# Performance work log

Hardware: AMD Instinct MI355X
Metric: run time of the kernel (lower is better)

The kernel has to match this reference:

```python
import jax, jax.numpy as jnp
import numpy as np

N = 100000   # nodes per graph-batch side
E = 1280000  # directed edges
G = 256      # graphs per batch
F_IN, HID, EMB = 64, 128, 64
BN_EPS = 1e-5


def setup_inputs() -> dict:
    key = jax.random.key(0)
    ks = jax.random.split(key, 24)
    inp = {}
    inp["x1"] = jax.random.normal(ks[0], (N, F_IN), dtype=jnp.float32)
    inp["x2"] = jax.random.normal(ks[1], (N, F_IN), dtype=jnp.float32)
    inp["edge_index1"] = jax.random.randint(ks[2], (2, E), 0, N, dtype=jnp.int64)
    inp["edge_index2"] = jax.random.randint(ks[3], (2, E), 0, N, dtype=jnp.int64)
    inp["batch1"] = jnp.sort(jax.random.randint(ks[4], (N,), 0, G, dtype=jnp.int64))
    inp["batch2"] = jnp.sort(jax.random.randint(ks[5], (N,), 0, G, dtype=jnp.int64))
    # shared (siamese) encoder parameters: 3 GIN layers (Linear+BN), final linear
    dims = [(F_IN, HID), (HID, HID), (HID, HID)]
    for i, (di, do) in enumerate(dims, 1):
        inp[f"W{i}"] = jax.random.normal(ks[5 + i], (di, do), dtype=jnp.float32) * (1.0 / np.sqrt(di))
        inp[f"b{i}"] = jnp.zeros((do,), dtype=jnp.float32)
        inp[f"g{i}"] = jnp.ones((do,), dtype=jnp.float32)   # BN gamma
        inp[f"be{i}"] = jnp.zeros((do,), dtype=jnp.float32)  # BN beta
    inp["Wf"] = jax.random.normal(ks[10], (HID, EMB), dtype=jnp.float32) * (1.0 / np.sqrt(HID))
    inp["bf"] = jnp.zeros((EMB,), dtype=jnp.float32)
    # classifier: Linear(EMB, HID//2) -> ReLU -> Linear(HID//2, 1) -> Sigmoid
    inp["Wc1"] = jax.random.normal(ks[11], (EMB, HID // 2), dtype=jnp.float32) * (1.0 / np.sqrt(EMB))
    inp["bc1"] = jnp.zeros((HID // 2,), dtype=jnp.float32)
    inp["Wc2"] = jax.random.normal(ks[12], (HID // 2, 1), dtype=jnp.float32) * (1.0 / np.sqrt(HID // 2))
    inp["bc2"] = jnp.zeros((1,), dtype=jnp.float32)
    return inp


def _gin_layer(x, src, dst, W, b, g, be):
    # GINConv eps=0: agg = x + sum_{j->i} x_j ; MLP = Linear -> BatchNorm1d -> ReLU
    agg = x + jax.ops.segment_sum(x[src], dst, num_segments=N)
    h = agg @ W + b
    mu = jnp.mean(h, axis=0)
    var = jnp.var(h, axis=0)
    h = (h - mu) * jax.lax.rsqrt(var + BN_EPS) * g + be
    return jax.nn.relu(h)  # MLP ReLU; outer .relu() in forward is idempotent


def _encode(x, edge_index, batch, Ws, bs, gs, bes, Wf, bf):
    src, dst = edge_index[0], edge_index[1]
    for W, b, g, be in zip(Ws, bs, gs, bes):
        x = _gin_layer(x, src, dst, W, b, g, be)
    # global_mean_pool
    sums = jax.ops.segment_sum(x, batch, num_segments=G)
    cnt = jax.ops.segment_sum(jnp.ones((N,), x.dtype), batch, num_segments=G)
    pooled = sums / jnp.maximum(cnt, 1.0)[:, None]
    return pooled @ Wf + bf


def reference(x1, edge_index1, batch1, x2, edge_index2, batch2,
              W1, b1, g1, be1, W2, b2, g2, be2, W3, b3, g3, be3,
              Wf, bf, Wc1, bc1, Wc2, bc2):
    Ws, bs, gs, bes = (W1, W2, W3), (b1, b2, b3), (g1, g2, g3), (be1, be2, be3)
    v1 = _encode(x1, edge_index1, batch1, Ws, bs, gs, bes, Wf, bf)
    v2 = _encode(x2, edge_index2, batch2, Ws, bs, gs, bes, Wf, bf)
    diff = jnp.abs(v1 - v2)
    h = jax.nn.relu(diff @ Wc1 + bc1)
    return jax.nn.sigmoid(h @ Wc2 + bc2)  # [G, 1]
```

## Files before the change

### kernel.cpp

```cpp
#include <hip/hip_runtime.h>
#include <hip/hip_bf16.h>
#include <math.h>

#define NN 100000
#define NE 1280000
#define NG 256
#define HID 128
#define EMB 64
#define BN_EPS 1e-5f
#define SB 1024
#define SNB ((NN + SB - 1) / SB)
#define GBLK 25000
#define NBG 1563
#define PART ((NN + 7) / 8)
#define FCH 2048
#define NCH (NE / FCH)

typedef __attribute__((ext_vector_type(8))) __bf16 bf16x8;
typedef __attribute__((ext_vector_type(4))) float f32x4;

__device__ __forceinline__ float bf2f(unsigned int u) { return __uint_as_float(u << 16); }
__device__ __forceinline__ unsigned int f2b(float f) {
    unsigned int u = __float_as_uint(f);
    return (u + 0x7fffu + ((u >> 16) & 1u)) >> 16;
}

__global__ void detect_i64_kernel(const void* __restrict__ ei, int* __restrict__ flag) {
    if (threadIdx.x == 0 && blockIdx.x == 0) {
        const unsigned long long* p = (const unsigned long long*)ei;
        int is64 = 1;
        #pragma unroll
        for (int i = 0; i < 16; ++i)
            if (p[i] >= (1ull << 32)) is64 = 0;
        *flag = is64;
    }
}

__device__ __forceinline__ int load_idx(const void* p, int i, bool is64) {
    return is64 ? (int)((const long long*)p)[i] : ((const int*)p)[i];
}

__global__ __launch_bounds__(256) void convert_x(const float* __restrict__ x1,
                                                 const float* __restrict__ x2,
                                                 ushort* __restrict__ o1,
                                                 ushort* __restrict__ o2) {
    const int per = NN * 16;
    const int i = blockIdx.x * 256 + threadIdx.x;
    const int side = i >= per;
    const int j = i - side * per;
    const float4 v = ((const float4*)(side ? x2 : x1))[j];
    ushort4 o;
    o.x = (ushort)f2b(v.x); o.y = (ushort)f2b(v.y);
    o.z = (ushort)f2b(v.z); o.w = (ushort)f2b(v.w);
    ((ushort4*)(side ? o2 : o1))[j] = o;
}

__global__ __launch_bounds__(256) void prep_weights(const float* __restrict__ W1,
                                                    const float* __restrict__ W2,
                                                    const float* __restrict__ W3,
                                                    ushort* __restrict__ T1,
                                                    ushort* __restrict__ T2,
                                                    ushort* __restrict__ T3) {
    const int i = blockIdx.x * 256 + threadIdx.x;
    if (i < 8192) {
        const int k = i >> 7, c = i & 127;
        T1[c * 64 + k] = (ushort)f2b(W1[i]);
    } else if (i < 24576) {
        const int j = i - 8192, k = j >> 7, c = j & 127;
        T2[c * 128 + k] = (ushort)f2b(W2[j]);
    } else if (i < 40960) {
        const int j = i - 24576, k = j >> 7, c = j & 127;
        T3[c * 128 + k] = (ushort)f2b(W3[j]);
    }
}

__global__ __launch_bounds__(256) void csr_hist2(const void* __restrict__ e1,
                                                 const void* __restrict__ e2,
                                                 int* __restrict__ degA,
                                                 int* __restrict__ degB,
                                                 const int* __restrict__ flag) {
    const bool is64 = (*flag != 0);
    const int i = blockIdx.x * 256 + threadIdx.x;
    if (i < 2 * NE) {
        const int side = i >= NE;
        const int j = i - side * NE;
        atomicAdd(&(side ? degB : degA)[load_idx(side ? e2 : e1, NE + j, is64)], 1);
    }
}

__global__ __launch_bounds__(256) void scan_block_sums2(const int* __restrict__ degA,
                                                        const int* __restrict__ degB,
                                                        int* __restrict__ bsum) {
    const int side = blockIdx.x >= SNB;
    const int bx = blockIdx.x - side * SNB;
    const int* deg = side ? degB : degA;
    const int t = threadIdx.x;
    const int base = bx * SB + t * 4;
    int s = 0;
    #pragma unroll
    for (int k = 0; k < 4; ++k) {
        const int i = base + k;
        if (i < NN) s += deg[i];
    }
    __shared__ int red[256];
    red[t] = s;
    __syncthreads();
    for (int off = 128; off > 0; off >>= 1) {
        if (t < off) red[t] += red[t + off];
        __syncthreads();
    }
    if (t == 0) bsum[side * 128 + bx] = red[0];
}

__global__ __launch_bounds__(128) void scan_bsums2(const int* __restrict__ bsum,
                                                   int* __restrict__ boff,
                                                   int* __restrict__ rpA,
                                                   int* __restrict__ rpB) {
    const int side = blockIdx.x;
    __shared__ int s[128];
    const int t = threadIdx.x;
    s[t] = (t < SNB) ? bsum[side * 128 + t] : 0;
    __syncthreads();
    for (int off = 1; off < 128; off <<= 1) {
        const int v = (t >= off) ? s[t - off] : 0;
        __syncthreads();
        s[t] += v;
        __syncthreads();
    }
    boff[side * 128 + t] = (t == 0) ? 0 : s[t - 1];
    if (t == 0) (side ? rpB : rpA)[NN] = s[SNB - 1];
}

__global__ __launch_bounds__(256) void scan_fill2(const int* __restrict__ degA,
                                                  const int* __restrict__ degB,
                                                  const int* __restrict__ boff,
                                                  int* __restrict__ rpA,
                                                  int* __restrict__ rpB,
                                                  int* __restrict__ curA,
                                                  int* __restrict__ curB) {
    const int side = blockIdx.x >= SNB;
    const int bx = blockIdx.x - side * SNB;
    const int* deg = side ? degB : degA;
    int* rowptr = side ? rpB : rpA;
    int* cursor = side ? curB : curA;
    const int t = threadIdx.x;
    const int base = bx * SB + t * 4;
    int v[4], s = 0;
    #pragma unroll
    for (int k = 0; k < 4; ++k) {
        const int i = base + k;
        v[k] = (i < NN) ? deg[i] : 0;
        s += v[k];
    }
    __shared__ int red[256];
    red[t] = s;
    __syncthreads();
    for (int off = 1; off < 256; off <<= 1) {
        const int x = (t >= off) ? red[t - off] : 0;
        __syncthreads();
        red[t] += x;
        __syncthreads();
    }
    int run = boff[side * 128 + bx] + ((t == 0) ? 0 : red[t - 1]);
    #pragma unroll
    for (int k = 0; k < 4; ++k) {
        const int i = base + k;
        if (i < NN) {
            rowptr[i] = run;
            cursor[i] = run;
            run += v[k];
        }
    }
}

__global__ __launch_bounds__(256) void csr_fill_part(const void* __restrict__ e1,
                                                     const void* __restrict__ e2,
                                                     int* __restrict__ curA,
                                                     int* __restrict__ curB,
                                                     int* __restrict__ colA,
                                                     int* __restrict__ colB,
                                                     const int* __restrict__ flag) {
    const bool is64 = (*flag != 0);
    const int g = blockIdx.x & 7;
    const int q = blockIdx.x >> 3;
    const int side = q >= NCH;
    const int chunk = q - side * NCH;
    const void* __restrict__ e = side ? e2 : e1;
    int* __restrict__ cur = side ? curB : curA;
    int* __restrict__ col = side ? colB : colA;
    const int lo = g * PART;
    const int hi = min(lo + PART, NN);
    const int base = chunk * FCH;
    for (int i = base + threadIdx.x; i < base + FCH; i += 256) {
        const int d = load_idx(e, NE + i, is64);
        if (d >= lo && d < hi) {
            const int pos = atomicAdd(&cur[d], 1);
            col[pos] = load_idx(e, i, is64);
        }
    }
}

struct GatherArgs {
    const ushort *xA, *xB;
    const int *rpA, *rpB, *colA, *colB;
    const float *stA, *stB;
    const float *gamma, *beta;
    ushort *oA, *oB;
};

template<int F, bool BN>
__global__ __launch_bounds__(256) void gather16(GatherArgs a) {
    const int side = blockIdx.x >= GBLK;
    const int bx = blockIdx.x - side * GBLK;
    const ushort* __restrict__ x = side ? a.xB : a.xA;
    const int* __restrict__ rowptr = side ? a.rpB : a.rpA;
    const int* __restrict__ col = side ? a.colB : a.colA;
    ushort* __restrict__ out = side ? a.oB : a.oA;

    const int node = (bx * 256 + threadIdx.x) >> 6;
    const int lane = threadIdx.x & 63;
    if (node >= NN) return;
    const int beg = rowptr[node], end = rowptr[node + 1];

    if (F == 64) {
        float acc = bf2f(x[node * 64 + lane]);
        int e = beg;
        for (; e + 3 < end; e += 4) {
            const int s0 = col[e], s1 = col[e + 1], s2 = col[e + 2], s3 = col[e + 3];
            acc += bf2f(x[s0 * 64 + lane]) + bf2f(x[s1 * 64 + lane])
                 + bf2f(x[s2 * 64 + lane]) + bf2f(x[s3 * 64 + lane]);
        }
        for (; e < end; ++e) acc += bf2f(x[col[e] * 64 + lane]);
        out[node * 64 + lane] = (ushort)f2b(acc);
    } else {
        float cax = 1.f, cay = 1.f, cbx = 0.f, cby = 0.f;
        if (BN) {
            const float* st = side ? a.stB : a.stA;
            const int c0 = lane * 2, c1 = c0 + 1;
            const float inv_n = 1.f / (float)NN;
            const float mu0 = st[c0] * inv_n, mu1 = st[c1] * inv_n;
            const float v0 = st[128 + c0] * inv_n - mu0 * mu0;
            const float v1 = st[128 + c1] * inv_n - mu1 * mu1;
            cax = a.gamma[c0] * rsqrtf(v0 + BN_EPS);
            cay = a.gamma[c1] * rsqrtf(v1 + BN_EPS);
            cbx = fmaf(-mu0, cax, a.beta[c0]);
            cby = fmaf(-mu1, cay, a.beta[c1]);
        }
        #define LD(s) (*(const unsigned int*)&x[(s) * 128 + lane * 2])
        #define FX(u) (BN ? fmaxf(fmaf(bf2f((u) & 0xffffu), cax, cbx), 0.f) : bf2f((u) & 0xffffu))
        #define FY(u) (BN ? fmaxf(fmaf(bf2f((u) >> 16),    cay, cby), 0.f) : bf2f((u) >> 16))
        const unsigned int u0 = LD(node);
        float ax = FX(u0), ay = FY(u0);
        int e = beg;
        for (; e + 3 < end; e += 4) {
            const unsigned int ua = LD(col[e]);
            const unsigned int ub = LD(col[e + 1]);
            const unsigned int uc = LD(col[e + 2]);
            const unsigned int ud = LD(col[e + 3]);
            ax += FX(ua) + FX(ub) + FX(uc) + FX(ud);
            ay += FY(ua) + FY(ub) + FY(uc) + FY(ud);
        }
        for (; e < end; ++e) {
            const unsigned int u = LD(col[e]);
            ax += FX(u); ay += FY(u);
        }
        #undef LD
        #undef FX
        #undef FY
        *(unsigned int*)&out[node * 128 + lane * 2] = f2b(ax) | (f2b(ay) << 16);
    }
}

struct GemmArgs {
    const ushort *mA, *mB;
    const ushort *WT;
    const float *bias;
    ushort *cA, *cB;
    float *stA, *stB;
};

template<int FIN>
__global__ __launch_bounds__(256) void gemm_mfma(GemmArgs g) {
    constexpr int FP = FIN + 8;
    constexpr int CPR = FIN / 8;
    const int side = blockIdx.x >= NBG;
    const int bx = blockIdx.x - side * NBG;
    const ushort* __restrict__ M = side ? g.mB : g.mA;
    ushort* __restrict__ C = side ? g.cB : g.cA;
    float* __restrict__ stats = side ? g.stB : g.stA;

    __shared__ ushort sh[64 * 136 + 128 * FP];
    ushort* Ml = sh;
    ushort* Wl = sh + 64 * 136;

    const int t = threadIdx.x;
    const int w = t >> 6;
    const int l = t & 63;
    const int lr = l & 15;
    const int lg = l >> 4;
    const int r0 = bx * 64;

    #pragma unroll
    for (int it = 0; it < (64 * CPR) / 256; ++it) {
        const int cid = it * 256 + t;
        const int row = cid / CPR, cc = (cid % CPR) * 8;
        const int r = r0 + row;
        uint4 v = make_uint4(0u, 0u, 0u, 0u);
        if (r < NN) v = *(const uint4*)&M[(size_t)r * FIN + cc];
        *(uint4*)&Ml[row * FP + cc] = v;
    }
    #pragma unroll
    for (int it = 0; it < (128 * CPR) / 256; ++it) {
        const int cid = it * 256 + t;
        const int c = cid / CPR, kk = (cid % CPR) * 8;
        *(uint4*)&Wl[c * FP + kk] = *(const uint4*)&g.WT[c * FIN + kk];
    }
    __syncthreads();

    f32x4 acc[4][2];
    #pragma unroll
    for (int fi = 0; fi < 4; ++fi)
        #pragma unroll
        for (int fj = 0; fj < 2; ++fj)
            acc[fi][fj] = (f32x4){0.f, 0.f, 0.f, 0.f};

    #pragma unroll
    for (int kc = 0; kc < FIN / 32; ++kc) {
        const int kb = kc * 32 + lg * 8;
        bf16x8 a[4], b[2];
        #pragma unroll
        for (int fi = 0; fi < 4; ++fi)
            a[fi] = *(const bf16x8*)&Ml[(fi * 16 + lr) * FP + kb];
        #pragma unroll
        for (int fj = 0; fj < 2; ++fj)
            b[fj] = *(const bf16x8*)&Wl[(w * 32 + fj * 16 + lr) * FP + kb];
        #pragma unroll
        for (int fi = 0; fi < 4; ++fi)
            #pragma unroll
            for (int fj = 0; fj < 2; ++fj)
                acc[fi][fj] = __builtin_amdgcn_mfma_f32_16x16x32_bf16(a[fi], b[fj], acc[fi][fj], 0, 0, 0);
    }
    __syncthreads();

    #pragma unroll
    for (int fj = 0; fj < 2; ++fj) {
        const float bv = g.bias[w * 32 + fj * 16 + lr];
        #pragma unroll
        for (int fi = 0; fi < 4; ++fi)
            #pragma unroll
            for (int j = 0; j < 4; ++j)
                acc[fi][fj][j] += bv;
    }
    #pragma unroll
    for (int fi = 0; fi < 4; ++fi)
        #pragma unroll
        for (int fj = 0; fj < 2; ++fj)
            #pragma unroll
            for (int j = 0; j < 4; ++j) {
                const int row = fi * 16 + lg * 4 + j;
                const int c = w * 32 + fj * 16 + lr;
                Ml[row * 136 + c] = (ushort)f2b(acc[fi][fj][j]);
            }
    __syncthreads();

    const int ry = t >> 4, c0 = (t & 15) * 8;
    float sc[8], qc[8];
    #pragma unroll
    for (int j = 0; j < 8; ++j) { sc[j] = 0.f; qc[j] = 0.f; }
    #pragma unroll
    for (int i = 0; i < 4; ++i) {
        const int rr = ry * 4 + i;
        const int r = r0 + rr;
        if (r < NN) {
            const uint4 pk = *(const uint4*)&Ml[rr * 136 + c0];
            const unsigned int uu[4] = {pk.x, pk.y, pk.z, pk.w};
            #pragma unroll
            for (int q = 0; q < 4; ++q) {
                const float e0 = bf2f(uu[q] & 0xffffu);
                const float e1 = bf2f(uu[q] >> 16);
                sc[2 * q] += e0;       sc[2 * q + 1] += e1;
                qc[2 * q] = fmaf(e0, e0, qc[2 * q]);
                qc[2 * q + 1] = fmaf(e1, e1, qc[2 * q + 1]);
            }
            *(uint4*)&C[(size_t)r * HID + c0] = pk;
        }
    }
    float* red = (float*)Wl;
    #pragma unroll
    for (int j = 0; j < 8; ++j) red[ry * 128 + c0 + j] = sc[j];
    __syncthreads();
    if (t < 128) {
        float a = 0.f;
        #pragma unroll
        for (int k = 0; k < 16; ++k) a += red[k * 128 + t];
        unsafeAtomicAdd(&stats[t], a);
    }
    __syncthreads();
    #pragma unroll
    for (int j = 0; j < 8; ++j) red[ry * 128 + c0 + j] = qc[j];
    __syncthreads();
    if (t < 128) {
        float a = 0.f;
        #pragma unroll
        for (int k = 0; k < 16; ++k) a += red[k * 128 + t];
        unsafeAtomicAdd(&stats[128 + t], a);
    }
}

struct PoolArgs {
    const ushort *hA, *hB;
    const void *btA, *btB;
    const float *stA, *stB;
    const float *gamma, *beta;
    float *pooled, *cnt;
    const int* flag;
};

__global__ __launch_bounds__(128) void pool16(PoolArgs p) {
    const int side = blockIdx.x >= NBG;
    const int bx = blockIdx.x - side * NBG;
    const ushort* __restrict__ h = side ? p.hB : p.hA;
    const void* __restrict__ batch = side ? p.btB : p.btA;
    const float* __restrict__ st = side ? p.stB : p.stA;
    float* pooled = p.pooled + side * NG * HID;
    float* cnt = p.cnt + side * NG;
    const bool is64 = (*p.flag != 0);
    const int c = threadIdx.x;

    const float inv_n = 1.f / (float)NN;
    const float mu = st[c] * inv_n;
    const float var = st[128 + c] * inv_n - mu * mu;
    const float ca = p.gamma[c] * rsqrtf(var + BN_EPS);
    const float cb = fmaf(-mu, ca, p.beta[c]);

    const int rbeg = bx * 64;
    if (rbeg >= NN) return;
    const int rend = min(rbeg + 64, NN);
    const int g0 = load_idx(batch, rbeg, is64);
    const int g1 = load_idx(batch, rend - 1, is64);
    if (g0 == g1) {
        float acc = 0.f;
        #pragma unroll 8
        for (int r = rbeg; r < rend; ++r)
            acc += fmaxf(fmaf(bf2f(h[r * HID + c]), ca, cb), 0.f);
        unsafeAtomicAdd(&pooled[g0 * HID + c], acc);
        if (c == 0) unsafeAtomicAdd(&cnt[g0], (float)(rend - rbeg));
        return;
    }
    int gprev = g0;
    float acc = 0.f; int run = 0;
    for (int r = rbeg; r < rend; ++r) {
        const int g = load_idx(batch, r, is64);
        if (g != gprev) {
            unsafeAtomicAdd(&pooled[gprev * HID + c], acc);
            if (c == 0) unsafeAtomicAdd(&cnt[gprev], (float)run);
            acc = 0.f; run = 0; gprev = g;
        }
        acc += fmaxf(fmaf(bf2f(h[r * HID + c]), ca, cb), 0.f);
        ++run;
    }
    unsafeAtomicAdd(&pooled[gprev * HID + c], acc);
    if (c == 0) unsafeAtomicAdd(&cnt[gprev], (float)run);
}

__global__ __launch_bounds__(64) void pool_proj(const float* __restrict__ pooled,
                                                const float* __restrict__ cnt,
                                                const float* __restrict__ Wf,
                                                const float* __restrict__ bf,
                                                float* __restrict__ v) {
    const int side = blockIdx.x >= NG;
    const int g = blockIdx.x - side * NG;
    const int c = threadIdx.x;
    const float* pp = pooled + side * NG * HID + g * HID;
    const float inv = 1.f / fmaxf(cnt[side * NG + g], 1.f);
    float acc = 0.f;
    for (int k = 0; k < HID; ++k) acc = fmaf(pp[k], Wf[k * EMB + c], acc);
    v[side * NG * EMB + g * EMB + c] = fmaf(acc, inv, bf[c]);
}

__global__ __launch_bounds__(256) void classifier(const float* __restrict__ v1,
                                                  const float* __restrict__ v2,
                                                  const float* __restrict__ Wc1,
                                                  const float* __restrict__ bc1,
                                                  const float* __restrict__ Wc2,
                                                  const float* __restrict__ bc2,
                                                  float* __restrict__ out) {
    const int g = threadIdx.x;
    if (g >= NG) return;
    float d[EMB];
    #pragma unroll
    for (int c = 0; c < EMB; ++c) d[c] = fabsf(v1[g * EMB + c] - v2[g * EMB + c]);
    float o = bc2[0];
    for (int j = 0; j < 32; ++j) {
        float h = bc1[j];
        #pragma unroll
        for (int c = 0; c < EMB; ++c) h = fmaf(d[c], Wc1[c * 32 + j], h);
        h = fmaxf(h, 0.f);
        o = fmaf(h, Wc2[j], o);
    }
    out[g] = 1.f / (1.f + expf(-o));
}

extern "C" void kernel_launch(void* const* d_in, const int* in_sizes, int n_in,
                              void* d_out, int out_size, void* d_ws, size_t ws_size,
                              hipStream_t stream) {
    const float* x1 = (const float*)d_in[0];
    const float* x2 = (const float*)d_in[1];
    const void* ei1 = d_in[2];
    const void* ei2 = d_in[3];
    const void* bt1 = d_in[4];
    const void* bt2 = d_in[5];
    const float* W[3]  = {(const float*)d_in[6],  (const float*)d_in[10], (const float*)d_in[14]};
    const float* bb[3] = {(const float*)d_in[7],  (const float*)d_in[11], (const float*)d_in[15]};
    const float* gg[3] = {(const float*)d_in[8],  (const float*)d_in[12], (const float*)d_in[16]};
    const float* be[3] = {(const float*)d_in[9],  (const float*)d_in[13], (const float*)d_in[17]};
    const float* Wf  = (const float*)d_in[18];
    const float* bfv = (const float*)d_in[19];
    const float* Wc1 = (const float*)d_in[20];
    const float* bc1 = (const float*)d_in[21];
    const float* Wc2 = (const float*)d_in[22];
    const float* bc2 = (const float*)d_in[23];

    char* cur = (char*)d_ws;
    auto alloc = [&](size_t bytes) -> void* {
        void* p = cur;
        cur += (bytes + 255) & ~(size_t)255;
        return p;
    };
    ushort* P0 = (ushort*)alloc((size_t)NN * HID * 2);
    ushort* P1 = (ushort*)alloc((size_t)NN * HID * 2);
    ushort* Q0 = (ushort*)alloc((size_t)NN * HID * 2);
    ushort* Q1 = (ushort*)alloc((size_t)NN * HID * 2);
    int* deg2   = (int*)alloc((size_t)2 * NN * 4);
    int* rpA    = (int*)alloc((size_t)(NN + 1) * 4);
    int* rpB    = (int*)alloc((size_t)(NN + 1) * 4);
    int* curA   = (int*)alloc((size_t)NN * 4);
    int* curB   = (int*)alloc((size_t)NN * 4);
    int* bsum   = (int*)alloc(256 * 4);
    int* boff   = (int*)alloc(256 * 4);
    int* colA   = (int*)alloc((size_t)NE * 4);
    int* colB   = (int*)alloc((size_t)NE * 4);
    int* flag   = (int*)alloc(64);
    ushort* WT1 = (ushort*)alloc(128 * 64 * 2);
    ushort* WT2 = (ushort*)alloc(128 * 128 * 2);
    ushort* WT3 = (ushort*)alloc(128 * 128 * 2);
    float* zreg = (float*)alloc((size_t)(6 * 256 + 2 * NG * HID + 2 * NG) * 4);
    float* stats  = zreg;
    float* pooled = stats + 6 * 256;
    float* cnt    = pooled + 2 * NG * HID;
    float* vv     = (float*)alloc((size_t)2 * NG * EMB * 4);
    int* degA = deg2, *degB = deg2 + NN;

    hipMemsetAsync(deg2, 0, (size_t)2 * NN * 4, stream);
    hipMemsetAsync(zreg, 0, (size_t)(6 * 256 + 2 * NG * HID + 2 * NG) * 4, stream);
    detect_i64_kernel<<<1, 64, 0, stream>>>(ei1, flag);
    convert_x<<<(2 * NN * 16) / 256, 256, 0, stream>>>(x1, x2, P0, P1);
    prep_weights<<<160, 256, 0, stream>>>(W[0], W[1], W[2], WT1, WT2, WT3);

    const int EB2 = (2 * NE + 255) / 256;
    csr_hist2<<<EB2, 256, 0, stream>>>(ei1, ei2, degA, degB, flag);
    scan_block_sums2<<<2 * SNB, 256, 0, stream>>>(degA, degB, bsum);
    scan_bsums2<<<2, 128, 0, stream>>>(bsum, boff, rpA, rpB);
    scan_fill2<<<2 * SNB, 256, 0, stream>>>(degA, degB, boff, rpA, rpB, curA, curB);
    csr_fill_part<<<8 * 2 * NCH, 256, 0, stream>>>(ei1, ei2, curA, curB, colA, colB, flag);

    float* st0A = stats + 0 * 256, *st0B = stats + 1 * 256;
    float* st1A = stats + 2 * 256, *st1B = stats + 3 * 256;
    float* st2A = stats + 4 * 256, *st2B = stats + 5 * 256;

    {
        GatherArgs a = {P0, P1, rpA, rpB, colA, colB, nullptr, nullptr, nullptr, nullptr, Q0, Q1};
        gather16<64, false><<<2 * GBLK, 256, 0, stream>>>(a);
        GemmArgs g = {Q0, Q1, WT1, bb[0], P0, P1, st0A, st0B};
        gemm_mfma<64><<<2 * NBG, 256, 0, stream>>>(g);
    }
    {
        GatherArgs a = {P0, P1, rpA, rpB, colA, colB, st0A, st0B, gg[0], be[0], Q0, Q1};
        gather16<128, true><<<2 * GBLK, 256, 0, stream>>>(a);
        GemmArgs g = {Q0, Q1, WT2, bb[1], Q0, Q1, st1A, st1B};
        gemm_mfma<128><<<2 * NBG, 256, 0, stream>>>(g);
    }
    {
        GatherArgs a = {Q0, Q1, rpA, rpB, colA, colB, st1A, st1B, gg[1], be[1], P0, P1};
        gather16<128, true><<<2 * GBLK, 256, 0, stream>>>(a);
        GemmArgs g = {P0, P1, WT3, bb[2], P0, P1, st2A, st2B};
        gemm_mfma<128><<<2 * NBG, 256, 0, stream>>>(g);
    }
    {
        PoolArgs p = {P0, P1, bt1, bt2, st2A, st2B, gg[2], be[2], pooled, cnt, flag};
        pool16<<<2 * NBG, 128, 0, stream>>>(p);
    }
    pool_proj<<<2 * NG, 64, 0, stream>>>(pooled, cnt, Wf, bfv, vv);
    classifier<<<1, 256, 0, stream>>>(vv, vv + NG * EMB, Wc1, bc1, Wc2, bc2, (float*)d_out);
}
```

Measured before the change: 992.3 us.

## Reorder GIN layers to transform before aggregating and interleave blocks across XCDs

Layers 2 and 3 now apply BN+ReLU and the linear transform first, then aggregate neighbours (gather_post), relying on linearity (sum then W equals W then sum). The bias is dropped because batch norm cancels it. BN statistics are computed in the gather_post pass, and the standalone gathers are remapped so each XCD processes one side. The reorder replaces the separate BN-apply gather with one fused into the GEMM load, but the stats now come from the aggregated output, which changes where the rounding happens.

```diff
diff --git a/kernel.cpp b/kernel.cpp
--- a/kernel.cpp
+++ b/kernel.cpp
@@ -10,8 +10,8 @@
 #define BN_EPS 1e-5f
 #define SB 1024
 #define SNB ((NN + SB - 1) / SB)
-#define GBLK 25000
 #define NBG 1563
+#define NB4 25000
 #define PART ((NN + 7) / 8)
 #define FCH 2048
 #define NCH (NE / FCH)
@@ -200,18 +200,16 @@
     }
 }
 
-struct GatherArgs {
+struct G64Args {
     const ushort *xA, *xB;
     const int *rpA, *rpB, *colA, *colB;
-    const float *stA, *stB;
-    const float *gamma, *beta;
     ushort *oA, *oB;
 };
 
-template<int F, bool BN>
-__global__ __launch_bounds__(256) void gather16(GatherArgs a) {
-    const int side = blockIdx.x >= GBLK;
-    const int bx = blockIdx.x - side * GBLK;
+__global__ __launch_bounds__(256) void gather64k(G64Args a) {
+    const int xcd = blockIdx.x & 7;
+    const int side = xcd >> 2;
+    const int bx = (blockIdx.x >> 3) * 4 + (xcd & 3);
     const ushort* __restrict__ x = side ? a.xB : a.xA;
     const int* __restrict__ rowptr = side ? a.rpB : a.rpA;
     const int* __restrict__ col = side ? a.colB : a.colA;
@@ -221,65 +219,93 @@
     const int lane = threadIdx.x & 63;
     if (node >= NN) return;
     const int beg = rowptr[node], end = rowptr[node + 1];
-
-    if (F == 64) {
-        float acc = bf2f(x[node * 64 + lane]);
+    float acc = bf2f(x[node * 64 + lane]);
+    int e = beg;
+    for (; e + 3 < end; e += 4) {
+        const int s0 = col[e], s1 = col[e + 1], s2 = col[e + 2], s3 = col[e + 3];
+        acc += bf2f(x[s0 * 64 + lane]) + bf2f(x[s1 * 64 + lane])
+             + bf2f(x[s2 * 64 + lane]) + bf2f(x[s3 * 64 + lane]);
+    }
+    for (; e < end; ++e) acc += bf2f(x[col[e] * 64 + lane]);
+    out[node * 64 + lane] = (ushort)f2b(acc);
+}
+
+struct GPostArgs {
+    const ushort *yA, *yB;
+    const int *rpA, *rpB, *colA, *colB;
+    ushort *rA, *rB;
+    float *stA, *stB;
+};
+
+__global__ __launch_bounds__(256) void gather_post(GPostArgs a) {
+    const int xcd = blockIdx.x & 7;
+    const int side = xcd >> 2;
+    const int bx = (blockIdx.x >> 3) * 4 + (xcd & 3);
+    if (bx >= NBG) return;
+    const ushort* __restrict__ y = side ? a.yB : a.yA;
+    const int* __restrict__ rowptr = side ? a.rpB : a.rpA;
+    const int* __restrict__ col = side ? a.colB : a.colA;
+    ushort* __restrict__ r = side ? a.rB : a.rA;
+    float* __restrict__ stats = side ? a.stB : a.stA;
+
+    const int t = threadIdx.x;
+    const int w = t >> 6, l = t & 63;
+    const int c2 = l * 2;
+    float s0 = 0.f, s1 = 0.f, q0 = 0.f, q1 = 0.f;
+
+    for (int i = 0; i < 16; ++i) {
+        const int node = bx * 64 + w * 16 + i;
+        if (node >= NN) break;
+        const int beg = rowptr[node], end = rowptr[node + 1];
+        const unsigned int u0 = *(const unsigned int*)&y[(size_t)node * 128 + c2];
+        float ax = bf2f(u0 & 0xffffu), ay = bf2f(u0 >> 16);
         int e = beg;
         for (; e + 3 < end; e += 4) {
-            const int s0 = col[e], s1 = col[e + 1], s2 = col[e + 2], s3 = col[e + 3];
-            acc += bf2f(x[s0 * 64 + lane]) + bf2f(x[s1 * 64 + lane])
-                 + bf2f(x[s2 * 64 + lane]) + bf2f(x[s3 * 64 + lane]);
-        }
-        for (; e < end; ++e) acc += bf2f(x[col[e] * 64 + lane]);
-        out[node * 64 + lane] = (ushort)f2b(acc);
-    } else {
-        float cax = 1.f, cay = 1.f, cbx = 0.f, cby = 0.f;
-        if (BN) {
-            const float* st = side ? a.stB : a.stA;
-            const int c0 = lane * 2, c1 = c0 + 1;
-            const float inv_n = 1.f / (float)NN;
-            const float mu0 = st[c0] * inv_n, mu1 = st[c1] * inv_n;
-            const float v0 = st[128 + c0] * inv_n - mu0 * mu0;
-            const float v1 = st[128 + c1] * inv_n - mu1 * mu1;
-            cax = a.gamma[c0] * rsqrtf(v0 + BN_EPS);
-            cay = a.gamma[c1] * rsqrtf(v1 + BN_EPS);
-            cbx = fmaf(-mu0, cax, a.beta[c0]);
-            cby = fmaf(-mu1, cay, a.beta[c1]);
-        }
-        #define LD(s) (*(const unsigned int*)&x[(s) * 128 + lane * 2])
-        #define FX(u) (BN ? fmaxf(fmaf(bf2f((u) & 0xffffu), cax, cbx), 0.f) : bf2f((u) & 0xffffu))
-        #define FY(u) (BN ? fmaxf(fmaf(bf2f((u) >> 16),    cay, cby), 0.f) : bf2f((u) >> 16))
-        const unsigned int u0 = LD(node);
-        float ax = FX(u0), ay = FY(u0);
-        int e = beg;
-        for (; e + 3 < end; e += 4) {
-            const unsigned int ua = LD(col[e]);
-            const unsigned int ub = LD(col[e + 1]);
-            const unsigned int uc = LD(col[e + 2]);
-            const unsigned int ud = LD(col[e + 3]);
-            ax += FX(ua) + FX(ub) + FX(uc) + FX(ud);
-            ay += FY(ua) + FY(ub) + FY(uc) + FY(ud);
+            const int sa = col[e], sb = col[e + 1], sc = col[e + 2], sd = col[e + 3];
+            const unsigned int ua = *(const unsigned int*)&y[(size_t)sa * 128 + c2];
+            const unsigned int ub = *(const unsigned int*)&y[(size_t)sb * 128 + c2];
+            const unsigned int uc = *(const unsigned int*)&y[(size_t)sc * 128 + c2];
+            const unsigned int ud = *(const unsigned int*)&y[(size_t)sd * 128 + c2];
+            ax += bf2f(ua & 0xffffu) + bf2f(ub & 0xffffu) + bf2f(uc & 0xffffu) + bf2f(ud & 0xffffu);
+            ay += bf2f(ua >> 16) + bf2f(ub >> 16) + bf2f(uc >> 16) + bf2f(ud >> 16);
         }
         for (; e < end; ++e) {
-            const unsigned int u = LD(col[e]);
-            ax += FX(u); ay += FY(u);
-        }
-        #undef LD
-        #undef FX
-        #undef FY
-        *(unsigned int*)&out[node * 128 + lane * 2] = f2b(ax) | (f2b(ay) << 16);
+            const unsigned int u = *(const unsigned int*)&y[(size_t)col[e] * 128 + c2];
+            ax += bf2f(u & 0xffffu);
+            ay += bf2f(u >> 16);
+        }
+        const unsigned int pk = f2b(ax) | (f2b(ay) << 16);
+        *(unsigned int*)&r[(size_t)node * 128 + c2] = pk;
+        const float e0 = bf2f(pk & 0xffffu), e1 = bf2f(pk >> 16);
+        s0 += e0; s1 += e1;
+        q0 = fmaf(e0, e0, q0); q1 = fmaf(e1, e1, q1);
+    }
+
+    __shared__ float red[512];
+    red[w * 128 + c2] = s0; red[w * 128 + c2 + 1] = s1;
+    __syncthreads();
+    if (t < 128) {
+        const float v = red[t] + red[128 + t] + red[256 + t] + red[384 + t];
+        unsafeAtomicAdd(&stats[t], v);
+    }
+    __syncthreads();
+    red[w * 128 + c2] = q0; red[w * 128 + c2 + 1] = q1;
+    __syncthreads();
+    if (t < 128) {
+        const float v = red[t] + red[128 + t] + red[256 + t] + red[384 + t];
+        unsafeAtomicAdd(&stats[128 + t], v);
     }
 }
 
 struct GemmArgs {
     const ushort *mA, *mB;
     const ushort *WT;
-    const float *bias;
     ushort *cA, *cB;
     float *stA, *stB;
+    const float *gamma, *beta;
 };
 
-template<int FIN>
+template<int FIN, bool APPLY_BN, bool STATS>
 __global__ __launch_bounds__(256) void gemm_mfma(GemmArgs g) {
     constexpr int FP = FIN + 8;
     constexpr int CPR = FIN / 8;
@@ -300,6 +326,21 @@
     const int lg = l >> 4;
     const int r0 = bx * 64;
 
+    float ca[8], cb[8];
+    if (APPLY_BN) {
+        const float* __restrict__ st = stats;
+        const int cc = (t % CPR) * 8;
+        const float inv_n = 1.f / (float)NN;
+        #pragma unroll
+        for (int j = 0; j < 8; ++j) {
+            const int c = cc + j;
+            const float mu = st[c] * inv_n;
+            const float var = st[128 + c] * inv_n - mu * mu;
+            ca[j] = g.gamma[c] * rsqrtf(var + BN_EPS);
+            cb[j] = fmaf(-mu, ca[j], g.beta[c]);
+        }
+    }
+
     #pragma unroll
     for (int it = 0; it < (64 * CPR) / 256; ++it) {
         const int cid = it * 256 + t;
@@ -307,6 +348,17 @@
         const int r = r0 + row;
         uint4 v = make_uint4(0u, 0u, 0u, 0u);
         if (r < NN) v = *(const uint4*)&M[(size_t)r * FIN + cc];
+        if (APPLY_BN) {
+            unsigned int vv[4] = {v.x, v.y, v.z, v.w};
+            #pragma unroll
+            for (int q2 = 0; q2 < 4; ++q2) {
+                float e0 = bf2f(vv[q2] & 0xffffu), e1 = bf2f(vv[q2] >> 16);
+                e0 = fmaxf(fmaf(e0, ca[2 * q2], cb[2 * q2]), 0.f);
+                e1 = fmaxf(fmaf(e1, ca[2 * q2 + 1], cb[2 * q2 + 1]), 0.f);
+                vv[q2] = f2b(e0) | (f2b(e1) << 16);
+            }
+            v = make_uint4(vv[0], vv[1], vv[2], vv[3]);
+        }
         *(uint4*)&Ml[row * FP + cc] = v;
     }
     #pragma unroll
@@ -342,15 +394,6 @@
     }
     __syncthreads();
 
-    #pragma unroll
-    for (int fj = 0; fj < 2; ++fj) {
-        const float bv = g.bias[w * 32 + fj * 16 + lr];
-        #pragma unroll
-        for (int fi = 0; fi < 4; ++fi)
-            #pragma unroll
-            for (int j = 0; j < 4; ++j)
-                acc[fi][fj][j] += bv;
-    }
     #pragma unroll
     for (int fi = 0; fi < 4; ++fi)
         #pragma unroll
@@ -365,45 +408,51 @@
 
     const int ry = t >> 4, c0 = (t & 15) * 8;
     float sc[8], qc[8];
-    #pragma unroll
-    for (int j = 0; j < 8; ++j) { sc[j] = 0.f; qc[j] = 0.f; }
+    if (STATS) {
+        #pragma unroll
+        for (int j = 0; j < 8; ++j) { sc[j] = 0.f; qc[j] = 0.f; }
+    }
     #pragma unroll
     for (int i = 0; i < 4; ++i) {
         const int rr = ry * 4 + i;
         const int r = r0 + rr;
         if (r < NN) {
             const uint4 pk = *(const uint4*)&Ml[rr * 136 + c0];
-            const unsigned int uu[4] = {pk.x, pk.y, pk.z, pk.w};
-            #pragma unroll
-            for (int q = 0; q < 4; ++q) {
-                const float e0 = bf2f(uu[q] & 0xffffu);
-                const float e1 = bf2f(uu[q] >> 16);
-                sc[2 * q] += e0;       sc[2 * q + 1] += e1;
-                qc[2 * q] = fmaf(e0, e0, qc[2 * q]);
-                qc[2 * q + 1] = fmaf(e1, e1, qc[2 * q + 1]);
+            if (STATS) {
+                const unsigned int uu[4] = {pk.x, pk.y, pk.z, pk.w};
+                #pragma unroll
+                for (int q2 = 0; q2 < 4; ++q2) {
+                    const float e0 = bf2f(uu[q2] & 0xffffu);
+                    const float e1 = bf2f(uu[q2] >> 16);
+                    sc[2 * q2] += e0;       sc[2 * q2 + 1] += e1;
+                    qc[2 * q2] = fmaf(e0, e0, qc[2 * q2]);
+                    qc[2 * q2 + 1] = fmaf(e1, e1, qc[2 * q2 + 1]);
+                }
             }
             *(uint4*)&C[(size_t)r * HID + c0] = pk;
         }
     }
-    float* red = (float*)Wl;
-    #pragma unroll
-    for (int j = 0; j < 8; ++j) red[ry * 128 + c0 + j] = sc[j];
-    __syncthreads();
-    if (t < 128) {
-        float a = 0.f;
-        #pragma unroll
-        for (int k = 0; k < 16; ++k) a += red[k * 128 + t];
-        unsafeAtomicAdd(&stats[t], a);
-    }
-    __syncthreads();
-    #pragma unroll
-    for (int j = 0; j < 8; ++j) red[ry * 128 + c0 + j] = qc[j];
-    __syncthreads();
-    if (t < 128) {
-        float a = 0.f;
-        #pragma unroll
-        for (int k = 0; k < 16; ++k) a += red[k * 128 + t];
-        unsafeAtomicAdd(&stats[128 + t], a);
+    if (STATS) {
+        float* red = (float*)Wl;
+        #pragma unroll
+        for (int j = 0; j < 8; ++j) red[ry * 128 + c0 + j] = sc[j];
+        __syncthreads();
+        if (t < 128) {
+            float a = 0.f;
+            #pragma unroll
+            for (int k = 0; k < 16; ++k) a += red[k * 128 + t];
+            unsafeAtomicAdd(&stats[t], a);
+        }
+        __syncthreads();
+        #pragma unroll
+        for (int j = 0; j < 8; ++j) red[ry * 128 + c0 + j] = qc[j];
+        __syncthreads();
+        if (t < 128) {
+            float a = 0.f;
+            #pragma unroll
+            for (int k = 0; k < 16; ++k) a += red[k * 128 + t];
+            unsafeAtomicAdd(&stats[128 + t], a);
+        }
     }
 }
 
@@ -511,7 +560,6 @@
     const void* bt1 = d_in[4];
     const void* bt2 = d_in[5];
     const float* W[3]  = {(const float*)d_in[6],  (const float*)d_in[10], (const float*)d_in[14]};
-    const float* bb[3] = {(const float*)d_in[7],  (const float*)d_in[11], (const float*)d_in[15]};
     const float* gg[3] = {(const float*)d_in[8],  (const float*)d_in[12], (const float*)d_in[16]};
     const float* be[3] = {(const float*)d_in[9],  (const float*)d_in[13], (const float*)d_in[17]};
     const float* Wf  = (const float*)d_in[18];
@@ -564,30 +612,32 @@
     scan_fill2<<<2 * SNB, 256, 0, stream>>>(degA, degB, boff, rpA, rpB, curA, curB);
     csr_fill_part<<<8 * 2 * NCH, 256, 0, stream>>>(ei1, ei2, curA, curB, colA, colB, flag);
 
-    float* st0A = stats + 0 * 256, *st0B = stats + 1 * 256;
-    float* st1A = stats + 2 * 256, *st1B = stats + 3 * 256;
-    float* st2A = stats + 4 * 256, *st2B = stats + 5 * 256;
+    float* st1A = stats + 0 * 256, *st1B = stats + 1 * 256;
+    float* st2A = stats + 2 * 256, *st2B = stats + 3 * 256;
+    float* st3A = stats + 4 * 256, *st3B = stats + 5 * 256;
+
+    const int GP = 8 * ((NBG + 3) / 4);
 
     {
-        GatherArgs a = {P0, P1, rpA, rpB, colA, colB, nullptr, nullptr, nullptr, nullptr, Q0, Q1};
-        gather16<64, false><<<2 * GBLK, 256, 0, stream>>>(a);
-        GemmArgs g = {Q0, Q1, WT1, bb[0], P0, P1, st0A, st0B};
-        gemm_mfma<64><<<2 * NBG, 256, 0, stream>>>(g);
+        G64Args a = {P0, P1, rpA, rpB, colA, colB, Q0, Q1};
+        gather64k<<<8 * (NB4 / 4), 256, 0, stream>>>(a);
+        GemmArgs g = {Q0, Q1, WT1, P0, P1, st1A, st1B, nullptr, nullptr};
+        gemm_mfma<64, false, true><<<2 * NBG, 256, 0, stream>>>(g);
     }
     {
-        GatherArgs a = {P0, P1, rpA, rpB, colA, colB, st0A, st0B, gg[0], be[0], Q0, Q1};
-        gather16<128, true><<<2 * GBLK, 256, 0, stream>>>(a);
-        GemmArgs g = {Q0, Q1, WT2, bb[1], Q0, Q1, st1A, st1B};
-        gemm_mfma<128><<<2 * NBG, 256, 0, stream>>>(g);
+        GemmArgs g = {P0, P1, WT2, Q0, Q1, st1A, st1B, gg[0], be[0]};
+        gemm_mfma<128, true, false><<<2 * NBG, 256, 0, stream>>>(g);
+        GPostArgs a = {Q0, Q1, rpA, rpB, colA, colB, P0, P1, st2A, st2B};
+        gather_post<<<GP, 256, 0, stream>>>(a);
     }
     {
-        GatherArgs a = {Q0, Q1, rpA, rpB, colA, colB, st1A, st1B, gg[1], be[1], P0, P1};
-        gather16<128, true><<<2 * GBLK, 256, 0, stream>>>(a);
-        GemmArgs g = {P0, P1, WT3, bb[2], P0, P1, st2A, st2B};
-        gemm_mfma<128><<<2 * NBG, 256, 0, stream>>>(g);
+        GemmArgs g = {P0, P1, WT3, Q0, Q1, st2A, st2B, gg[1], be[1]};
+        gemm_mfma<128, true, false><<<2 * NBG, 256, 0, stream>>>(g);
+        GPostArgs a = {Q0, Q1, rpA, rpB, colA, colB, P0, P1, st3A, st3B};
+        gather_post<<<GP, 256, 0, stream>>>(a);
     }
     {
-        PoolArgs p = {P0, P1, bt1, bt2, st2A, st2B, gg[2], be[2], pooled, cnt, flag};
+        PoolArgs p = {P0, P1, bt1, bt2, st3A, st3B, gg[2], be[2], pooled, cnt, flag};
         pool16<<<2 * NBG, 128, 0, stream>>>(p);
     }
     pool_proj<<<2 * NG, 64, 0, stream>>>(pooled, cnt, Wf, bfv, vv);
```

Result: faster. 931.0 us (-6.2%).
